# Kernel tuning notes

Hardware: AMD Instinct MI355X
Metric: run time of the kernel (lower is better)

## Reference

```python
import jax, jax.numpy as jnp
import numpy as np

EMBED_DIM = 64
D_STATE = 16
D_CONV = 4
EXPAND = 2
DT_RANK = 8
D_INNER = EXPAND * EMBED_DIM  # 128
B_, T_, H_, W_ = 4, 16, 16, 16


def _causal_dwconv(x, w, b):
    # x: (B, D, L), w: (D, 1, K) depthwise causal conv (left pad K-1), matches
    # torch conv1d(padding=K-1)[..., :L]
    K = w.shape[-1]
    y = jax.lax.conv_general_dilated(
        x, w, window_strides=(1,), padding=[(K - 1, 0)],
        feature_group_count=x.shape[1], dimension_numbers=('NCH', 'OIH', 'NCH'))
    return y + b[None, :, None]


def _selective_scan(u, delta, A, Bm, Cm, D):
    # u, delta: (B, d, L); A: (d, n); Bm, Cm: (B, n, L); D: (d,)
    dA = jnp.exp(jnp.einsum('bdl,dn->lbdn', delta, A))      # (L,B,d,n)
    dBu = jnp.einsum('bdl,bnl,bdl->lbdn', delta, Bm, u)     # (L,B,d,n)
    h0 = jnp.zeros(dA.shape[1:], dA.dtype)

    def step(h, xs):
        dA_t, dBu_t = xs
        h = dA_t * h + dBu_t
        return h, h

    _, hs = jax.lax.scan(step, h0, (dA, dBu))               # (L,B,d,n)
    y = jnp.einsum('lbdn,bnl->bdl', hs, Cm)
    return y + u * D[None, :, None]


def _mamba_branch(x, z, conv_w, conv_b, xproj_w, dtproj_w, dtproj_b, A_log, D):
    # x, z: (B, d_inner, L)
    x = jax.nn.silu(_causal_dwconv(x, conv_w, conv_b))
    x_dbl = jnp.einsum('bdl,ed->bel', x, xproj_w)           # e = dt_rank + 2*n
    dt = x_dbl[:, :DT_RANK]
    Bm = x_dbl[:, DT_RANK:DT_RANK + D_STATE]
    Cm = x_dbl[:, DT_RANK + D_STATE:]
    delta = jax.nn.softplus(jnp.einsum('brl,dr->bdl', dt, dtproj_w) + dtproj_b[None, :, None])
    A = -jnp.exp(A_log)
    y = _selective_scan(x, delta, A, Bm, Cm, D)
    return y * jax.nn.silu(z)


def _conv3d(x, w, b, pad):
    y = jax.lax.conv_general_dilated(
        x, w, window_strides=(1, 1, 1), padding=[(pad, pad)] * 3,
        dimension_numbers=('NCDHW', 'OIDHW', 'NCDHW'))
    return y + b[None, :, None, None, None]


def setup_inputs() -> dict:
    key = jax.random.key(0)
    ks = jax.random.split(key, 24)
    s = 0.02
    d, n, r, K, C = D_INNER, D_STATE, DT_RANK, D_CONV, EMBED_DIM
    inp = {
        'x': jax.random.normal(ks[0], (B_, C, T_, H_, W_), jnp.float32),
        'in_proj_w': jax.random.normal(ks[1], (2 * d, C), jnp.float32) * s,
        'conv_w': jax.random.normal(ks[2], (d, 1, K), jnp.float32) * s,
        'conv_b': jnp.zeros((d,), jnp.float32),
        'xproj_w': jax.random.normal(ks[3], (r + 2 * n, d), jnp.float32) * s,
        'dtproj_w': jax.random.normal(ks[4], (d, r), jnp.float32) * s,
        'dtproj_b': jax.random.normal(ks[5], (d,), jnp.float32) * s,
        'A_log': jnp.tile(jnp.log(jnp.arange(1, n + 1, dtype=jnp.float32))[None, :], (d, 1)),
        'D': jnp.ones((d,), jnp.float32),
        'conv_w_b': jax.random.normal(ks[6], (d, 1, K), jnp.float32) * s,
        'conv_b_b': jnp.zeros((d,), jnp.float32),
        'xproj_w_b': jax.random.normal(ks[7], (r + 2 * n, d), jnp.float32) * s,
        'dtproj_w_b': jax.random.normal(ks[8], (d, r), jnp.float32) * s,
        'dtproj_b_b': jax.random.normal(ks[9], (d,), jnp.float32) * s,
        'A_b_log': jnp.tile(jnp.log(jnp.arange(1, n + 1, dtype=jnp.float32))[None, :], (d, 1)),
        'D_b': jnp.ones((d,), jnp.float32),
        'out_proj_w': jax.random.normal(ks[10], (C, d), jnp.float32) * s,
        'proj_w': jax.random.normal(ks[11], (C, C, 3, 3, 3), jnp.float32) * s,
        'proj_b': jnp.zeros((C,), jnp.float32),
        'norm_w': jax.random.normal(ks[12], (C, C, 1, 1, 1), jnp.float32) * s,
        'norm_b': jnp.zeros((C,), jnp.float32),
    }
    return inp


def reference(x, in_proj_w, conv_w, conv_b, xproj_w, dtproj_w, dtproj_b, A_log, D,
              conv_w_b, conv_b_b, xproj_w_b, dtproj_w_b, dtproj_b_b, A_b_log, D_b,
              out_proj_w, proj_w, proj_b, norm_w, norm_b):
    residual = x
    B, C, T, H, W = x.shape
    # SpectralPriority scan: b c t h w -> b c (h w t)
    seq = x.transpose(0, 1, 3, 4, 2).reshape(B, C, H * W * T)
    # bimamba v2
    xz = jnp.einsum('bcl,ec->bel', seq, in_proj_w)          # (B, 2*d_inner, L)
    x_f, z_f = xz[:, :D_INNER], xz[:, D_INNER:]
    y_f = _mamba_branch(x_f, z_f, conv_w, conv_b, xproj_w, dtproj_w, dtproj_b, A_log, D)
    xz_r = jnp.flip(xz, -1)
    x_b, z_b = xz_r[:, :D_INNER], xz_r[:, D_INNER:]
    y_b = _mamba_branch(x_b, z_b, conv_w_b, conv_b_b, xproj_w_b, dtproj_w_b, dtproj_b_b, A_b_log, D_b)
    out = y_f + jnp.flip(y_b, -1)                           # (B, d_inner, L)
    out = jnp.einsum('bdl,cd->blc', out, out_proj_w)        # (B, L, C)
    x_recon = out.reshape(B, C, T, H, W)
    x3 = _conv3d(x_recon, proj_w, proj_b, pad=1)
    return _conv3d(x3 + residual, norm_w, norm_b, pad=0)
```

## Files before the change

kernel.cpp:

```cpp
#include <hip/hip_runtime.h>


#define NL 4096

typedef unsigned short u16;
typedef unsigned int u32;
typedef __attribute__((ext_vector_type(8))) short bf16x8;
typedef __attribute__((ext_vector_type(4))) float f32x4;

__device__ __forceinline__ float siluf_(float x) {
  return x * __builtin_amdgcn_rcpf(1.f + __expf(-x));
}
__device__ __forceinline__ float softplusf_(float x) {
  return (x > 20.f) ? x : __logf(1.f + __expf(x));
}
__device__ __forceinline__ u16 f2bf(float f) {
  u32 u = __float_as_uint(f);
  u += 0x7fffu + ((u >> 16) & 1u);
  return (u16)(u >> 16);
}

__device__ __forceinline__ float rowsum16_(float p) {
  int q;
  q = __builtin_amdgcn_mov_dpp(__float_as_int(p), 0x121, 0xf, 0xf, false);
  p += __int_as_float(q);
  q = __builtin_amdgcn_mov_dpp(__float_as_int(p), 0x122, 0xf, 0xf, false);
  p += __int_as_float(q);
  q = __builtin_amdgcn_mov_dpp(__float_as_int(p), 0x124, 0xf, 0xf, false);
  p += __int_as_float(q);
  q = __builtin_amdgcn_mov_dpp(__float_as_int(p), 0x128, 0xf, 0xf, false);
  p += __int_as_float(q);
  return p;
}

#define OXZ  0u
#define OUCF 1048576u
#define OUCB 1572864u
#define ODLF 2424832u
#define ODLB 2949120u
#define OYF  3473408u
#define OYB  3997696u
#define OO   4521984u
#define OO2  5046272u
#define PER_B 5570560u

#define NCH 64
#define CL  64
#define WB1 110592u

__global__ __launch_bounds__(256) void kxz(
    const float* __restrict__ x, const float* __restrict__ wip,
    float* __restrict__ ws, int b0) {
  int bi = blockIdx.y, gb = b0 + bi;
  float* s = ws + (size_t)bi * PER_B;
  int bid = blockIdx.x;
  int h = bid >> 4, w = bid & 15;
  int tid = threadIdx.x;
  __shared__ float xs[64][16];
  for (int i = tid; i < 1024; i += 256) {
    int c = i >> 4, t = i & 15;
    xs[c][t] = x[(size_t)(gb * 64 + c) * NL + t * 256 + h * 16 + w];
  }
  __syncthreads();
  int e = tid;
  float acc[16];
#pragma unroll
  for (int t = 0; t < 16; ++t) acc[t] = 0.f;
  for (int c = 0; c < 64; ++c) {
    float wv = wip[e * 64 + c];
#pragma unroll
    for (int t = 0; t < 16; ++t) acc[t] = fmaf(wv, xs[c][t], acc[t]);
  }
  float4* dst = (float4*)(s + OXZ + (size_t)e * NL + h * 256 + w * 16);
#pragma unroll
  for (int q = 0; q < 4; ++q)
    dst[q] = make_float4(acc[q * 4], acc[q * 4 + 1], acc[q * 4 + 2], acc[q * 4 + 3]);
}

__global__ __launch_bounds__(256) void k2prep(
    const float* __restrict__ cwf, const float* __restrict__ cbf,
    const float* __restrict__ xpf, const float* __restrict__ dtwf,
    const float* __restrict__ dtbf,
    const float* __restrict__ cwb, const float* __restrict__ cbb,
    const float* __restrict__ xpb, const float* __restrict__ dtwb,
    const float* __restrict__ dtbb,
    float* __restrict__ ws) {
  int bi = blockIdx.y;
  float* s = ws + (size_t)bi * PER_B;
  int bx = blockIdx.x;
  int lt = bx >> 1, dir = bx & 1;
  int l0 = lt * 32;
  int lout0 = dir ? (127 - lt) * 32 : l0;
  int tid = threadIdx.x;

  __shared__ float pool[128 * 40];
  __shared__ u16 uct[32][136];
  float (*X)[40] = (float(*)[40])pool;

  for (int i = tid; i < 128 * 38; i += 256) {
    int d = i / 38, j = i - d * 38;
    int l = l0 - 3 + j;
    X[d][j] = (l >= 0 && l < NL) ? s[OXZ + (size_t)d * NL + l] : 0.f;
  }
  __syncthreads();

  const float* cw = dir ? cwb : cwf;
  const float* cb = dir ? cbb : cbf;
  float* ucg = s + (dir ? OUCB : OUCF);
  for (int i = tid; i < 128 * 32; i += 256) {
    int d = i >> 5, li = i & 31;
    float a = cb[d];
    if (dir == 0) {
#pragma unroll
      for (int k = 0; k < 4; ++k) a = fmaf(cw[d * 4 + k], X[d][li + k], a);
    } else {
#pragma unroll
      for (int k = 0; k < 4; ++k) a = fmaf(cw[d * 4 + k], X[d][37 - li - k], a);
    }
    a = siluf_(a);
    uct[li][d] = f2bf(a);
    ucg[(size_t)d * NL + lout0 + li] = a;
  }
  __syncthreads();

  float* xds = pool;
  {
    int wid = tid >> 6, lane = tid & 63;
    int n16 = lane & 15, kg = lane >> 4;
    const float* xp = dir ? xpb : xpf;
#pragma unroll
    for (int rep = 0; rep < 2; ++rep) {
      int id = wid + rep * 4;
      if (id < 6) {
        int et = id >> 1, lt2 = id & 1;
        f32x4 acc = {};
#pragma unroll
        for (int ks = 0; ks < 4; ++ks) {
          bf16x8 bfrag = *(const bf16x8*)&uct[lt2 * 16 + n16][ks * 32 + kg * 8];
          int e = et * 16 + n16;
          int ec = (e < 40) ? e : 39;
          const float* pa = xp + ec * 128 + ks * 32 + kg * 8;
          float4 a0 = *(const float4*)pa;
          float4 a1 = *(const float4*)(pa + 4);
          bf16x8 af;
          af[0] = (short)f2bf(a0.x); af[1] = (short)f2bf(a0.y);
          af[2] = (short)f2bf(a0.z); af[3] = (short)f2bf(a0.w);
          af[4] = (short)f2bf(a1.x); af[5] = (short)f2bf(a1.y);
          af[6] = (short)f2bf(a1.z); af[7] = (short)f2bf(a1.w);
          acc = __builtin_amdgcn_mfma_f32_16x16x32_bf16(af, bfrag, acc, 0, 0, 0);
        }
#pragma unroll
        for (int rg = 0; rg < 4; ++rg) {
          int e = et * 16 + kg * 4 + rg;
          if (e < 40) xds[e * 33 + lt2 * 16 + n16] = acc[rg];
        }
      }
    }
  }
  __syncthreads();

  const float* dtw = dir ? dtwb : dtwf;
  const float* dtb = dir ? dtbb : dtbf;
  float* dlg = s + (dir ? ODLB : ODLF);
  for (int i = tid; i < 128 * 32; i += 256) {
    int d = i >> 5, li = i & 31;
    float pre = dtb[d];
#pragma unroll
    for (int r = 0; r < 8; ++r)
      pre = fmaf(dtw[d * 8 + r], xds[r * 33 + li], pre);
    dlg[(size_t)d * NL + lout0 + li] = softplusf_(pre);
  }
  u16* bctp = (u16*)(s + OO2);
  for (int i = tid; i < 32 * 32; i += 256) {
    int li = i >> 5, k = i & 31;
    bctp[((size_t)dir * 4096 + lout0 + li) * 32 + k] = f2bf(xds[(8 + k) * 33 + li]);
  }
}

__global__ __launch_bounds__(256) void kscanA(
    const float* __restrict__ Alf, const float* __restrict__ Alb,
    float* __restrict__ ws) {
  int bi = blockIdx.y;
  float* s = ws + (size_t)bi * PER_B;
  int xid = blockIdx.x;
  int chunk = xid >> 4, dir = (xid >> 3) & 1, d8 = xid & 7;
  int tid = threadIdx.x;
  int wv = tid >> 6, lane = tid & 63;
  int n = lane & 15, g = lane >> 4;
  int d = d8 * 16 + wv * 4 + g;
  int l0 = chunk * CL;
  __shared__ float bl[CL * 16];
  {
    const u16* bctp = (const u16*)(s + OO2) + ((size_t)dir * 4096 + l0) * 32;
    for (int i = tid; i < CL * 16; i += 256) {
      int l = i >> 4, k = i & 15;
      bl[i] = __uint_as_float(((u32)bctp[l * 32 + k]) << 16);
    }
  }
  __syncthreads();
  const float* ucp = s + (dir ? OUCB : OUCF) + (size_t)d * NL + l0;
  const float* dlp = s + (dir ? ODLB : ODLF) + (size_t)d * NL + l0;
  const float* blB = bl + n;
  float A = -__expf((dir ? Alb : Alf)[d * 16 + n]);
  float P = 1.f, S = 0.f;
#pragma unroll
  for (int i0 = 0; i0 < CL; i0 += 8) {
    float4 dq0 = *(const float4*)(dlp + i0);
    float4 dq1 = *(const float4*)(dlp + i0 + 4);
    float4 uq0 = *(const float4*)(ucp + i0);
    float4 uq1 = *(const float4*)(ucp + i0 + 4);
    float dv[8] = {dq0.x, dq0.y, dq0.z, dq0.w, dq1.x, dq1.y, dq1.z, dq1.w};
    float uv[8] = {uq0.x, uq0.y, uq0.z, uq0.w, uq1.x, uq1.y, uq1.z, uq1.w};
#pragma unroll
    for (int j = 0; j < 8; ++j) {
      float dA = __expf(dv[j] * A);
      S = fmaf(dA, S, dv[j] * blB[(i0 + j) * 16] * uv[j]);
      P *= dA;
    }
  }
  size_t cidx = ((size_t)(chunk * 2 + dir) * 128 + d) * 16 + n;
  s[OO + cidx] = P;
  s[OO + 262144u + cidx] = S;
}

__global__ __launch_bounds__(256) void kscanC(
    const float* __restrict__ Alf, const float* __restrict__ Df,
    const float* __restrict__ Alb, const float* __restrict__ Db,
    float* __restrict__ ws) {
  int bi = blockIdx.y;
  float* s = ws + (size_t)bi * PER_B;
  int xid = blockIdx.x;
  int chunk = xid >> 4, dir = (xid >> 3) & 1, d8 = xid & 7;
  int tid = threadIdx.x;
  int wv = tid >> 6, lane = tid & 63;
  int n = lane & 15, g = lane >> 4;
  int d = d8 * 16 + wv * 4 + g;
  int l0 = chunk * CL;
  __shared__ float bl[CL * 32];
  __shared__ float ps[16][65];
  {
    const u16* bctp = (const u16*)(s + OO2) + ((size_t)dir * 4096 + l0) * 32;
    for (int i = tid; i < CL * 32; i += 256)
      bl[i] = __uint_as_float(((u32)bctp[i]) << 16);
  }
  __syncthreads();
  const float* ucp = s + (dir ? OUCB : OUCF) + (size_t)d * NL + l0;
  const float* dlp = s + (dir ? ODLB : ODLF) + (size_t)d * NL + l0;
  const float* blB = bl + n;
  float* ybase = s + (dir ? OYB : OYF);
  float A = -__expf((dir ? Alb : Alf)[d * 16 + n]);
  float Dv = (dir ? Db : Df)[d];
  float h = 0.f;
  {
    size_t stepi = (size_t)d * 16 + n;
#pragma unroll 4
    for (int c = 0; c < chunk; ++c) {
      size_t idx = ((size_t)(c * 2 + dir) * 128) * 16 + stepi;
      float pv = s[OO + idx], sv = s[OO + 262144u + idx];
      h = fmaf(pv, h, sv);
    }
  }
  int prow = wv * 4 + g;
#pragma unroll
  for (int i0 = 0; i0 < CL; i0 += 8) {
    float4 dq0 = *(const float4*)(dlp + i0);
    float4 dq1 = *(const float4*)(dlp + i0 + 4);
    float4 uq0 = *(const float4*)(ucp + i0);
    float4 uq1 = *(const float4*)(ucp + i0 + 4);
    float dv[8] = {dq0.x, dq0.y, dq0.z, dq0.w, dq1.x, dq1.y, dq1.z, dq1.w};
    float uv[8] = {uq0.x, uq0.y, uq0.z, uq0.w, uq1.x, uq1.y, uq1.z, uq1.w};
    float yv[8];
#pragma unroll
    for (int j = 0; j < 8; ++j) {
      float dA = __expf(dv[j] * A);
      h = fmaf(dA, h, dv[j] * blB[(i0 + j) * 32] * uv[j]);
      float p = rowsum16_(h * blB[(i0 + j) * 32 + 16]);
      yv[j] = fmaf(uv[j], Dv, p);
    }
    if (n == 0) {
#pragma unroll
      for (int j = 0; j < 8; ++j) ps[prow][i0 + j] = yv[j];
    }
  }
  __syncthreads();
  for (int i = tid; i < 16 * CL; i += 256) {
    int row = i >> 6, col = i & 63;
    ybase[(size_t)(d8 * 16 + row) * NL + l0 + col] = ps[row][col];
  }
}

__global__ __launch_bounds__(256) void koutg(
    const float* __restrict__ wout, float* __restrict__ ws) {
  int bi = blockIdx.y;
  float* s = ws + (size_t)bi * PER_B;
  int lt = blockIdx.x;
  int l0 = lt * 32;
  int tid = threadIdx.x;
  __shared__ u16 otb[32][136];
  for (int i = tid; i < 128 * 32; i += 256) {
    int d = i >> 5, li = i & 31;
    int l = l0 + li;
    float z = s[OXZ + (size_t)(128 + d) * NL + l];
    float v = s[OYF + (size_t)d * NL + l] + s[OYB + (size_t)d * NL + (NL - 1 - l)];
    otb[li][d] = f2bf(v * siluf_(z));
  }
  __syncthreads();
  int wid = tid >> 6, lane = tid & 63;
  int n16 = lane & 15, kg = lane >> 4;
  f32x4 acc[2] = {};
  const float* wr = wout + (size_t)(wid * 16 + n16) * 128 + kg * 8;
#pragma unroll
  for (int ks = 0; ks < 4; ++ks) {
    const float* pa = wr + ks * 32;
    float4 a0 = *(const float4*)pa;
    float4 a1 = *(const float4*)(pa + 4);
    bf16x8 af;
    af[0] = (short)f2bf(a0.x); af[1] = (short)f2bf(a0.y);
    af[2] = (short)f2bf(a0.z); af[3] = (short)f2bf(a0.w);
    af[4] = (short)f2bf(a1.x); af[5] = (short)f2bf(a1.y);
    af[6] = (short)f2bf(a1.z); af[7] = (short)f2bf(a1.w);
    bf16x8 b0 = *(const bf16x8*)&otb[n16][ks * 32 + kg * 8];
    bf16x8 b1 = *(const bf16x8*)&otb[16 + n16][ks * 32 + kg * 8];
    acc[0] = __builtin_amdgcn_mfma_f32_16x16x32_bf16(af, b0, acc[0], 0, 0, 0);
    acc[1] = __builtin_amdgcn_mfma_f32_16x16x32_bf16(af, b1, acc[1], 0, 0, 0);
  }
#pragma unroll
  for (int l2 = 0; l2 < 2; ++l2) {
    float4 st = make_float4(acc[l2][0], acc[l2][1], acc[l2][2], acc[l2][3]);
    *(float4*)&s[OO2 + (size_t)(l0 + l2 * 16 + n16) * 64 + wid * 16 + kg * 4] = st;
  }
}

__global__ __launch_bounds__(256) void kprepw(
    const float* __restrict__ pw, float* __restrict__ wdst) {
  int off = blockIdx.x;
  u16* wb = (u16*)wdst;
  int tid = threadIdx.x;
  for (int i = tid; i < 4096; i += 256) {
    int co = i >> 6, ci = i & 63;
    u16 v = f2bf(pw[(size_t)(co * 64 + ci) * 27 + off]);
#pragma unroll
    for (int xc = 0; xc < 8; ++xc)
      wb[(size_t)xc * WB1 + off * 4096 + i] = v;
  }
}

__global__ __launch_bounds__(256, 2) void kconv3(
    const float* __restrict__ pb, const float* __restrict__ nw,
    const float* __restrict__ nb, const float* __restrict__ xin,
    float* __restrict__ out, const u16* __restrict__ wb,
    float* __restrict__ ws, int b0) {
  int bi = blockIdx.y, gb = b0 + bi;
  float* s = ws + (size_t)bi * PER_B;
  int bx = blockIdx.x;
  int t = bx >> 3, hq = bx & 7;
  int h0 = hq * 2;
  int tid = threadIdx.x;
  const float* xr = s + OO2;

  __shared__ u16 Xs[3 * 4 * 18 * 72];
  float* cx = (float*)Xs;
  {
    u32* xz32 = (u32*)Xs;
    for (int i = tid; i < 3 * 4 * 18 * 72 / 2; i += 256) xz32[i] = 0u;
  }
  __syncthreads();
  {
    int ci = tid >> 2, wq = tid & 3;
#pragma unroll
    for (int rowc = 0; rowc < 12; ++rowc) {
      int tt = rowc >> 2, hh = rowc & 3;
      int ts = t + tt - 1, hs = h0 + hh - 1;
      if (ts < 0 || ts > 15 || hs < 0 || hs > 15) continue;
      float4 v = *(const float4*)(xr + (size_t)ci * NL + ts * 256 + hs * 16 + wq * 4);
      int rb = (tt * 4 + hh) * 18 + 1 + wq * 4;
      Xs[(rb + 0) * 72 + ci] = f2bf(v.x);
      Xs[(rb + 1) * 72 + ci] = f2bf(v.y);
      Xs[(rb + 2) * 72 + ci] = f2bf(v.z);
      Xs[(rb + 3) * 72 + ci] = f2bf(v.w);
    }
  }
  __syncthreads();

  int wid = tid >> 6, lane = tid & 63;
  int cq = wid;
  int n16 = lane & 15, kg = lane >> 4;
  f32x4 acc[2] = {};

  const u16* wbA = wb + (size_t)(bx & 7) * WB1 +
                   (size_t)(cq * 16 + n16) * 64 + kg * 8;
#pragma unroll
  for (int kt = 0; kt < 3; ++kt)
#pragma unroll
    for (int kh = 0; kh < 3; ++kh) {
#pragma unroll
      for (int kw = 0; kw < 3; ++kw) {
        int off = (kt * 3 + kh) * 3 + kw;
        const u16* pa = wbA + off * 4096;
#pragma unroll
        for (int st = 0; st < 2; ++st) {
          int kb = st * 32;
          bf16x8 a0 = *(const bf16x8*)(pa + kb);
#pragma unroll
          for (int l2 = 0; l2 < 2; ++l2) {
            int r = (kt * 4 + l2 + kh) * 18 + n16 + kw;
            bf16x8 b0 = *(const bf16x8*)(&Xs[r * 72 + kb + kg * 8]);
            acc[l2] = __builtin_amdgcn_mfma_f32_16x16x32_bf16(a0, b0, acc[l2], 0, 0, 0);
          }
        }
      }
    }
  __syncthreads();

#pragma unroll
  for (int l2 = 0; l2 < 2; ++l2) {
    int lp = l2 * 16 + n16;
    int lg = t * 256 + (h0 + l2) * 16 + n16;
#pragma unroll
    for (int rg = 0; rg < 4; ++rg) {
      int co = cq * 16 + kg * 4 + rg;
      cx[co * 33 + lp] = acc[l2][rg] + pb[co] +
                         xin[(size_t)(gb * 64 + co) * NL + lg];
    }
  }
  __syncthreads();

  {
    int co2 = tid >> 2, pq = tid & 3;
    float mac[8];
#pragma unroll
    for (int j = 0; j < 8; ++j) mac[j] = 0.f;
    for (int ci = 0; ci < 64; ci += 4) {
      float4 w4 = *(const float4*)&nw[co2 * 64 + ci];
      float wv[4] = {w4.x, w4.y, w4.z, w4.w};
#pragma unroll
      for (int cc = 0; cc < 4; ++cc) {
        const float* row = &cx[(ci + cc) * 33 + pq * 8];
        float4 a = *(const float4*)&row[0];
        float4 b = *(const float4*)&row[4];
        mac[0] = fmaf(wv[cc], a.x, mac[0]);  mac[1] = fmaf(wv[cc], a.y, mac[1]);
        mac[2] = fmaf(wv[cc], a.z, mac[2]);  mac[3] = fmaf(wv[cc], a.w, mac[3]);
        mac[4] = fmaf(wv[cc], b.x, mac[4]);  mac[5] = fmaf(wv[cc], b.y, mac[5]);
        mac[6] = fmaf(wv[cc], b.z, mac[6]);  mac[7] = fmaf(wv[cc], b.w, mac[7]);
      }
    }
    float bias = nb[co2];
    float4* dst = (float4*)(out + (size_t)(gb * 64 + co2) * NL +
                            t * 256 + h0 * 16 + pq * 8);
    dst[0] = make_float4(mac[0] + bias, mac[1] + bias, mac[2] + bias, mac[3] + bias);
    dst[1] = make_float4(mac[4] + bias, mac[5] + bias, mac[6] + bias, mac[7] + bias);
  }
}

extern "C" void kernel_launch(void* const* d_in, const int* in_sizes, int n_in,
                              void* d_out, int out_size, void* d_ws, size_t ws_size,
                              hipStream_t stream) {
  const float* x    = (const float*)d_in[0];
  const float* wip  = (const float*)d_in[1];
  const float* cwf  = (const float*)d_in[2];
  const float* cbf  = (const float*)d_in[3];
  const float* xpf  = (const float*)d_in[4];
  const float* dtwf = (const float*)d_in[5];
  const float* dtbf = (const float*)d_in[6];
  const float* Alf  = (const float*)d_in[7];
  const float* Df   = (const float*)d_in[8];
  const float* cwb  = (const float*)d_in[9];
  const float* cbb  = (const float*)d_in[10];
  const float* xpb  = (const float*)d_in[11];
  const float* dtwb = (const float*)d_in[12];
  const float* dtbb = (const float*)d_in[13];
  const float* Alb  = (const float*)d_in[14];
  const float* Db   = (const float*)d_in[15];
  const float* wout = (const float*)d_in[16];
  const float* pw   = (const float*)d_in[17];
  const float* pb   = (const float*)d_in[18];
  const float* nw   = (const float*)d_in[19];
  const float* nb   = (const float*)d_in[20];

  const size_t PER_B_BYTES = (size_t)PER_B * 4;
  const size_t WB_BYTES = 8u * WB1 * 2u;
  int bcnt;
  if (ws_size >= 4 * PER_B_BYTES + WB_BYTES) bcnt = 4;
  else if (ws_size >= PER_B_BYTES + WB_BYTES) bcnt = 1;
  else return;
  int passes = 4 / bcnt;

  float* ws = (float*)d_ws;
  float* wsW = ws + (size_t)bcnt * PER_B;
  kprepw<<<dim3(27), 256, 0, stream>>>(pw, wsW);
  for (int p = 0; p < passes; ++p) {
    int b0 = p * bcnt;
    kxz   <<<dim3(256, bcnt), 256, 0, stream>>>(x, wip, ws, b0);
    k2prep<<<dim3(256, bcnt), 256, 0, stream>>>(cwf, cbf, xpf, dtwf, dtbf,
                                                cwb, cbb, xpb, dtwb, dtbb, ws);
    kscanA<<<dim3(1024, bcnt), 256, 0, stream>>>(Alf, Alb, ws);
    kscanC<<<dim3(1024, bcnt), 256, 0, stream>>>(Alf, Df, Alb, Db, ws);
    koutg <<<dim3(128, bcnt), 256, 0, stream>>>(wout, ws);
    kconv3<<<dim3(128, bcnt), 256, 0, stream>>>(pb, nw, nb, x, (float*)d_out,
                                                (const u16*)wsW, ws, b0);
  }
}
```

Measured before the change: 257.8 us.

## Process two independent scan chunks per block to interleave recurrences

Each block of the chunked scan kernels now handles two chunks (c and c+32) at once, halving the grid to 512 blocks per batch. The two independent recurrence chains are interleaved to hide exp/FMA and DPP reduction latency. In kscanC, one pass over the chunk prefix yields both starting states. The cost is more registers and shared memory per block, and half as many blocks.

```diff
diff --git a/kernel.cpp b/kernel.cpp
--- a/kernel.cpp
+++ b/kernel.cpp
@@ -183,44 +183,62 @@
   int bi = blockIdx.y;
   float* s = ws + (size_t)bi * PER_B;
   int xid = blockIdx.x;
-  int chunk = xid >> 4, dir = (xid >> 3) & 1, d8 = xid & 7;
+  int c0 = xid >> 4, dir = (xid >> 3) & 1, d8 = xid & 7;
+  int c1 = c0 + 32;
   int tid = threadIdx.x;
   int wv = tid >> 6, lane = tid & 63;
   int n = lane & 15, g = lane >> 4;
   int d = d8 * 16 + wv * 4 + g;
-  int l0 = chunk * CL;
-  __shared__ float bl[CL * 16];
-  {
-    const u16* bctp = (const u16*)(s + OO2) + ((size_t)dir * 4096 + l0) * 32;
-    for (int i = tid; i < CL * 16; i += 256) {
-      int l = i >> 4, k = i & 15;
-      bl[i] = __uint_as_float(((u32)bctp[l * 32 + k]) << 16);
-    }
-  }
-  __syncthreads();
-  const float* ucp = s + (dir ? OUCB : OUCF) + (size_t)d * NL + l0;
-  const float* dlp = s + (dir ? ODLB : ODLF) + (size_t)d * NL + l0;
-  const float* blB = bl + n;
+  int l0a = c0 * CL, l0b = c1 * CL;
+  __shared__ float bl[2][CL * 16];
+  {
+    const u16* bctp = (const u16*)(s + OO2);
+    for (int i = tid; i < 2 * CL * 16; i += 256) {
+      int which = i >> 10, r = i & 1023;
+      int l = r >> 4, k = r & 15;
+      size_t lg = (size_t)dir * 4096 + (which ? l0b : l0a) + l;
+      bl[which][r] = __uint_as_float(((u32)bctp[lg * 32 + k]) << 16);
+    }
+  }
+  __syncthreads();
+  const float* ucpA = s + (dir ? OUCB : OUCF) + (size_t)d * NL + l0a;
+  const float* dlpA = s + (dir ? ODLB : ODLF) + (size_t)d * NL + l0a;
+  const float* ucpB = s + (dir ? OUCB : OUCF) + (size_t)d * NL + l0b;
+  const float* dlpB = s + (dir ? ODLB : ODLF) + (size_t)d * NL + l0b;
+  const float* blA = bl[0] + n;
+  const float* blBp = bl[1] + n;
   float A = -__expf((dir ? Alb : Alf)[d * 16 + n]);
-  float P = 1.f, S = 0.f;
+  float P0 = 1.f, S0 = 0.f, P1 = 1.f, S1 = 0.f;
 #pragma unroll
   for (int i0 = 0; i0 < CL; i0 += 8) {
-    float4 dq0 = *(const float4*)(dlp + i0);
-    float4 dq1 = *(const float4*)(dlp + i0 + 4);
-    float4 uq0 = *(const float4*)(ucp + i0);
-    float4 uq1 = *(const float4*)(ucp + i0 + 4);
-    float dv[8] = {dq0.x, dq0.y, dq0.z, dq0.w, dq1.x, dq1.y, dq1.z, dq1.w};
-    float uv[8] = {uq0.x, uq0.y, uq0.z, uq0.w, uq1.x, uq1.y, uq1.z, uq1.w};
+    float4 da0 = *(const float4*)(dlpA + i0);
+    float4 da1 = *(const float4*)(dlpA + i0 + 4);
+    float4 ua0 = *(const float4*)(ucpA + i0);
+    float4 ua1 = *(const float4*)(ucpA + i0 + 4);
+    float4 db0 = *(const float4*)(dlpB + i0);
+    float4 db1 = *(const float4*)(dlpB + i0 + 4);
+    float4 ub0 = *(const float4*)(ucpB + i0);
+    float4 ub1 = *(const float4*)(ucpB + i0 + 4);
+    float dvA[8] = {da0.x, da0.y, da0.z, da0.w, da1.x, da1.y, da1.z, da1.w};
+    float uvA[8] = {ua0.x, ua0.y, ua0.z, ua0.w, ua1.x, ua1.y, ua1.z, ua1.w};
+    float dvB[8] = {db0.x, db0.y, db0.z, db0.w, db1.x, db1.y, db1.z, db1.w};
+    float uvB[8] = {ub0.x, ub0.y, ub0.z, ub0.w, ub1.x, ub1.y, ub1.z, ub1.w};
 #pragma unroll
     for (int j = 0; j < 8; ++j) {
-      float dA = __expf(dv[j] * A);
-      S = fmaf(dA, S, dv[j] * blB[(i0 + j) * 16] * uv[j]);
-      P *= dA;
-    }
-  }
-  size_t cidx = ((size_t)(chunk * 2 + dir) * 128 + d) * 16 + n;
-  s[OO + cidx] = P;
-  s[OO + 262144u + cidx] = S;
+      float dA0 = __expf(dvA[j] * A);
+      S0 = fmaf(dA0, S0, dvA[j] * blA[(i0 + j) * 16] * uvA[j]);
+      P0 *= dA0;
+      float dA1 = __expf(dvB[j] * A);
+      S1 = fmaf(dA1, S1, dvB[j] * blBp[(i0 + j) * 16] * uvB[j]);
+      P1 *= dA1;
+    }
+  }
+  size_t cidx0 = ((size_t)(c0 * 2 + dir) * 128 + d) * 16 + n;
+  size_t cidx1 = ((size_t)(c1 * 2 + dir) * 128 + d) * 16 + n;
+  s[OO + cidx0] = P0;
+  s[OO + 262144u + cidx0] = S0;
+  s[OO + cidx1] = P1;
+  s[OO + 262144u + cidx1] = S1;
 }
 
 __global__ __launch_bounds__(256) void kscanC(
@@ -230,62 +248,92 @@
   int bi = blockIdx.y;
   float* s = ws + (size_t)bi * PER_B;
   int xid = blockIdx.x;
-  int chunk = xid >> 4, dir = (xid >> 3) & 1, d8 = xid & 7;
+  int c0 = xid >> 4, dir = (xid >> 3) & 1, d8 = xid & 7;
+  int c1 = c0 + 32;
   int tid = threadIdx.x;
   int wv = tid >> 6, lane = tid & 63;
   int n = lane & 15, g = lane >> 4;
   int d = d8 * 16 + wv * 4 + g;
-  int l0 = chunk * CL;
-  __shared__ float bl[CL * 32];
-  __shared__ float ps[16][65];
-  {
-    const u16* bctp = (const u16*)(s + OO2) + ((size_t)dir * 4096 + l0) * 32;
-    for (int i = tid; i < CL * 32; i += 256)
-      bl[i] = __uint_as_float(((u32)bctp[i]) << 16);
-  }
-  __syncthreads();
-  const float* ucp = s + (dir ? OUCB : OUCF) + (size_t)d * NL + l0;
-  const float* dlp = s + (dir ? ODLB : ODLF) + (size_t)d * NL + l0;
-  const float* blB = bl + n;
+  int l0a = c0 * CL, l0b = c1 * CL;
+  __shared__ float bl[2][CL * 32];
+  __shared__ float ps[2][16][65];
+  {
+    const u16* bctp = (const u16*)(s + OO2);
+    for (int i = tid; i < 2 * CL * 32; i += 256) {
+      int which = i >> 11, r = i & 2047;
+      size_t lg = (size_t)dir * 4096 + (which ? l0b : l0a);
+      bl[which][r] = __uint_as_float(((u32)bctp[lg * 32 + r]) << 16);
+    }
+  }
+  float h0 = 0.f, h1;
+  {
+    size_t stepi = (size_t)d * 16 + n;
+    float h = 0.f;
+#pragma unroll 4
+    for (int c = 0; c < c0; ++c) {
+      size_t idx = ((size_t)(c * 2 + dir) * 128) * 16 + stepi;
+      h = fmaf(s[OO + idx], h, s[OO + 262144u + idx]);
+    }
+    h0 = h;
+#pragma unroll 4
+    for (int c = c0; c < c1; ++c) {
+      size_t idx = ((size_t)(c * 2 + dir) * 128) * 16 + stepi;
+      h = fmaf(s[OO + idx], h, s[OO + 262144u + idx]);
+    }
+    h1 = h;
+  }
+  __syncthreads();
+  const float* ucpA = s + (dir ? OUCB : OUCF) + (size_t)d * NL + l0a;
+  const float* dlpA = s + (dir ? ODLB : ODLF) + (size_t)d * NL + l0a;
+  const float* ucpB = s + (dir ? OUCB : OUCF) + (size_t)d * NL + l0b;
+  const float* dlpB = s + (dir ? ODLB : ODLF) + (size_t)d * NL + l0b;
+  const float* blA = bl[0] + n;
+  const float* blBp = bl[1] + n;
   float* ybase = s + (dir ? OYB : OYF);
   float A = -__expf((dir ? Alb : Alf)[d * 16 + n]);
   float Dv = (dir ? Db : Df)[d];
-  float h = 0.f;
-  {
-    size_t stepi = (size_t)d * 16 + n;
-#pragma unroll 4
-    for (int c = 0; c < chunk; ++c) {
-      size_t idx = ((size_t)(c * 2 + dir) * 128) * 16 + stepi;
-      float pv = s[OO + idx], sv = s[OO + 262144u + idx];
-      h = fmaf(pv, h, sv);
-    }
-  }
   int prow = wv * 4 + g;
 #pragma unroll
   for (int i0 = 0; i0 < CL; i0 += 8) {
-    float4 dq0 = *(const float4*)(dlp + i0);
-    float4 dq1 = *(const float4*)(dlp + i0 + 4);
-    float4 uq0 = *(const float4*)(ucp + i0);
-    float4 uq1 = *(const float4*)(ucp + i0 + 4);
-    float dv[8] = {dq0.x, dq0.y, dq0.z, dq0.w, dq1.x, dq1.y, dq1.z, dq1.w};
-    float uv[8] = {uq0.x, uq0.y, uq0.z, uq0.w, uq1.x, uq1.y, uq1.z, uq1.w};
-    float yv[8];
+    float4 da0 = *(const float4*)(dlpA + i0);
+    float4 da1 = *(const float4*)(dlpA + i0 + 4);
+    float4 ua0 = *(const float4*)(ucpA + i0);
+    float4 ua1 = *(const float4*)(ucpA + i0 + 4);
+    float4 db0 = *(const float4*)(dlpB + i0);
+    float4 db1 = *(const float4*)(dlpB + i0 + 4);
+    float4 ub0 = *(const float4*)(ucpB + i0);
+    float4 ub1 = *(const float4*)(ucpB + i0 + 4);
+    float dvA[8] = {da0.x, da0.y, da0.z, da0.w, da1.x, da1.y, da1.z, da1.w};
+    float uvA[8] = {ua0.x, ua0.y, ua0.z, ua0.w, ua1.x, ua1.y, ua1.z, ua1.w};
+    float dvB[8] = {db0.x, db0.y, db0.z, db0.w, db1.x, db1.y, db1.z, db1.w};
+    float uvB[8] = {ub0.x, ub0.y, ub0.z, ub0.w, ub1.x, ub1.y, ub1.z, ub1.w};
+    float yv0[8], yv1[8];
 #pragma unroll
     for (int j = 0; j < 8; ++j) {
-      float dA = __expf(dv[j] * A);
-      h = fmaf(dA, h, dv[j] * blB[(i0 + j) * 32] * uv[j]);
-      float p = rowsum16_(h * blB[(i0 + j) * 32 + 16]);
-      yv[j] = fmaf(uv[j], Dv, p);
+      float dA0 = __expf(dvA[j] * A);
+      h0 = fmaf(dA0, h0, dvA[j] * blA[(i0 + j) * 32] * uvA[j]);
+      float p0 = rowsum16_(h0 * blA[(i0 + j) * 32 + 16]);
+      yv0[j] = fmaf(uvA[j], Dv, p0);
+      float dA1 = __expf(dvB[j] * A);
+      h1 = fmaf(dA1, h1, dvB[j] * blBp[(i0 + j) * 32] * uvB[j]);
+      float p1 = rowsum16_(h1 * blBp[(i0 + j) * 32 + 16]);
+      yv1[j] = fmaf(uvB[j], Dv, p1);
     }
     if (n == 0) {
 #pragma unroll
-      for (int j = 0; j < 8; ++j) ps[prow][i0 + j] = yv[j];
-    }
-  }
-  __syncthreads();
-  for (int i = tid; i < 16 * CL; i += 256) {
-    int row = i >> 6, col = i & 63;
-    ybase[(size_t)(d8 * 16 + row) * NL + l0 + col] = ps[row][col];
+      for (int j = 0; j < 8; ++j) {
+        ps[0][prow][i0 + j] = yv0[j];
+        ps[1][prow][i0 + j] = yv1[j];
+      }
+    }
+  }
+  __syncthreads();
+  for (int i = tid; i < 2 * 16 * CL; i += 256) {
+    int which = i >> 10;
+    int r = i & 1023;
+    int row = r >> 6, col = r & 63;
+    ybase[(size_t)(d8 * 16 + row) * NL + (which ? l0b : l0a) + col] =
+        ps[which][row][col];
   }
 }
 
@@ -493,8 +541,8 @@
     kxz   <<<dim3(256, bcnt), 256, 0, stream>>>(x, wip, ws, b0);
     k2prep<<<dim3(256, bcnt), 256, 0, stream>>>(cwf, cbf, xpf, dtwf, dtbf,
                                                 cwb, cbb, xpb, dtwb, dtbb, ws);
-    kscanA<<<dim3(1024, bcnt), 256, 0, stream>>>(Alf, Alb, ws);
-    kscanC<<<dim3(1024, bcnt), 256, 0, stream>>>(Alf, Df, Alb, Db, ws);
+    kscanA<<<dim3(512, bcnt), 256, 0, stream>>>(Alf, Alb, ws);
+    kscanC<<<dim3(512, bcnt), 256, 0, stream>>>(Alf, Df, Alb, Db, ws);
     koutg <<<dim3(128, bcnt), 256, 0, stream>>>(wout, ws);
     kconv3<<<dim3(128, bcnt), 256, 0, stream>>>(pb, nw, nb, x, (float*)d_out,
                                                 (const u16*)wsW, ws, b0);
```

After: 260.8 us. About the same (+1.1%).
